# Kernel optimization log

Measured on AMD Instinct MI355X. Metric: run time of the kernel, lower is better.

## Reference

```python
import jax, jax.numpy as jnp
import numpy as np
import math

D = 128
LAMBDA_INIT = 0.8 - 0.6 * math.exp(-0.3 * 1)  # depth=1


def _clin(xr, xi, wr, wi, br, bi):
    # complex linear: (xr + i xi) @ (wr + i wi)^T + (br + i bi)
    o_r = jnp.einsum('bhsd,od->bhso', xr, wr) - jnp.einsum('bhsd,od->bhso', xi, wi) + br
    o_i = jnp.einsum('bhsd,od->bhso', xr, wi) + jnp.einsum('bhsd,od->bhso', xi, wr) + bi
    return o_r, o_i


def setup_inputs() -> dict:
    key = jax.random.key(0)
    ks = jax.random.split(key, 32)
    B, H, S = 1, 12, 1024
    shp = (B, H, S, D)
    inp = {}
    names = ['q_r', 'q_i', 'k_r', 'k_i', 'v_r', 'v_i', 'pe_q_r', 'pe_q_i', 'pe_k_r', 'pe_k_i']
    for i, n in enumerate(names):
        inp[n] = jax.random.normal(ks[i], shp, dtype=jnp.float32)
    std = 1.0 / math.sqrt(D)
    inp['qw_r'] = jax.random.normal(ks[10], (2 * D, D), jnp.float32) * std
    inp['qw_i'] = jax.random.normal(ks[11], (2 * D, D), jnp.float32) * std
    inp['qb_r'] = jnp.zeros((2 * D,), jnp.float32)
    inp['qb_i'] = jnp.zeros((2 * D,), jnp.float32)
    for j, p in enumerate(['k', 'v', 'g', 'o']):
        inp[p + 'w_r'] = jax.random.normal(ks[12 + 2 * j], (D, D), jnp.float32) * std
        inp[p + 'w_i'] = jax.random.normal(ks[13 + 2 * j], (D, D), jnp.float32) * std
        inp[p + 'b_r'] = jnp.zeros((D,), jnp.float32)
        inp[p + 'b_i'] = jnp.zeros((D,), jnp.float32)
    inp['lq1'] = jax.random.normal(ks[20], (D,), jnp.float32) * 0.1
    inp['lk1'] = jax.random.normal(ks[21], (D,), jnp.float32) * 0.1
    inp['lq2'] = jax.random.normal(ks[22], (D,), jnp.float32) * 0.1
    inp['lk2'] = jax.random.normal(ks[23], (D,), jnp.float32) * 0.1
    inp['sub_w'] = jnp.ones((2 * D,), jnp.float32)
    return inp


def _forward(q_r, q_i, k_r, k_i, v_r, v_i, pe_q_r, pe_q_i, pe_k_r, pe_k_i,
             qw_r, qw_i, qb_r, qb_i, kw_r, kw_i, kb_r, kb_i,
             vw_r, vw_i, vb_r, vb_i, gw_r, gw_i, gb_r, gb_i,
             ow_r, ow_i, ob_r, ob_i, lq1, lk1, lq2, lk2, sub_w):
    scale = D ** (-0.5)
    qp_r, qp_i = _clin(q_r, q_i, qw_r, qw_i, qb_r, qb_i)   # [B,H,S,2D]
    kp_r, kp_i = _clin(k_r, k_i, kw_r, kw_i, kb_r, kb_i)   # [B,H,S,D]
    vp_r, vp_i = _clin(v_r, v_i, vw_r, vw_i, vb_r, vb_i)
    qp_r = qp_r + jnp.concatenate([pe_q_r, pe_q_r], axis=-1)
    qp_i = qp_i + jnp.concatenate([pe_q_i, pe_q_i], axis=-1)
    kp_r = kp_r + pe_k_r
    kp_i = kp_i + pe_k_i
    q1_r, q2_r = jnp.split(qp_r, 2, axis=-1)
    q1_i, q2_i = jnp.split(qp_i, 2, axis=-1)

    def attn_w(qr, qi):
        s_r = jnp.einsum('bhqd,bhkd->bhqk', qr, kp_r) + jnp.einsum('bhqd,bhkd->bhqk', qi, kp_i)
        s_i = jnp.einsum('bhqd,bhkd->bhqk', qi, kp_r) - jnp.einsum('bhqd,bhkd->bhqk', qr, kp_i)
        mag = jnp.sqrt(s_r ** 2 + s_i ** 2 + 1e-8) * scale
        return jax.nn.softmax(mag.astype(jnp.float32), axis=-1).astype(s_r.dtype)

    w1 = attn_w(q1_r, q1_i)
    w2 = attn_w(q2_r, q2_i)
    a1_r = jnp.einsum('bhqk,bhkd->bhqd', w1, vp_r)
    a1_i = jnp.einsum('bhqk,bhkd->bhqd', w1, vp_i)
    a2_r = jnp.einsum('bhqk,bhkd->bhqd', w2, vp_r)
    a2_i = jnp.einsum('bhqk,bhkd->bhqd', w2, vp_i)
    cat_r = jnp.concatenate([a1_r, a2_r], axis=-1)
    cat_i = jnp.concatenate([a1_i, a2_i], axis=-1)
    rms = jnp.sqrt(jnp.mean(cat_r ** 2 + cat_i ** 2, axis=-1, keepdims=True) + 1e-5)
    cat_r = cat_r / rms * sub_w
    cat_i = cat_i / rms * sub_w
    a1_r, a2_r = jnp.split(cat_r, 2, axis=-1)
    a1_i, a2_i = jnp.split(cat_i, 2, axis=-1)
    lam1 = jnp.exp(jnp.sum(lq1 * lk1))
    lam2 = jnp.exp(jnp.sum(lq2 * lk2))
    lam = jax.nn.sigmoid(lam1 - lam2 + LAMBDA_INIT)
    out_r = a1_r - lam * a2_r
    out_i = a1_i - lam * a2_i
    g_r, g_i = _clin(q_r, q_i, gw_r, gw_i, gb_r, gb_i)
    out_r, out_i = g_r * out_r - g_i * out_i, g_r * out_i + g_i * out_r
    out_r, out_i = _clin(out_r, out_i, ow_r, ow_i, ob_r, ob_i)
    return out_r, out_i


def reference(q_r, q_i, k_r, k_i, v_r, v_i, pe_q_r, pe_q_i, pe_k_r, pe_k_i,
              qw_r, qw_i, qb_r, qb_i, kw_r, kw_i, kb_r, kb_i,
              vw_r, vw_i, vb_r, vb_i, gw_r, gw_i, gb_r, gb_i,
              ow_r, ow_i, ob_r, ob_i, lq1, lk1, lq2, lk2, sub_w):
    return _forward(q_r, q_i, k_r, k_i, v_r, v_i, pe_q_r, pe_q_i, pe_k_r, pe_k_i,
                    qw_r, qw_i, qb_r, qb_i, kw_r, kw_i, kb_r, kb_i,
                    vw_r, vw_i, vb_r, vb_i, gw_r, gw_i, gb_r, gb_i,
                    ow_r, ow_i, ob_r, ob_i, lq1, lk1, lq2, lk2, sub_w)
```

## Files before the change

kernel.cpp:

```cpp
#include <hip/hip_runtime.h>
#include <math.h>

#define H 12
#define S 1024
#define D 128
#define NROWS (H * S)

typedef __attribute__((ext_vector_type(8))) _Float16 f16x8;
typedef __attribute__((ext_vector_type(4))) float f32x4;
typedef __attribute__((ext_vector_type(4))) int i32x4;

__device__ __forceinline__ short f2h(float f) {
    _Float16 h = (_Float16)f;
    return __builtin_bit_cast(short, h);
}
__device__ __forceinline__ f16x8 fneg8(f16x8 v) {
    i32x4 u = __builtin_bit_cast(i32x4, v);
    u ^= (int)0x80008000;
    return __builtin_bit_cast(f16x8, u);
}

#define WS_QP_R   0ULL
#define WS_QP_I   6291456ULL
#define WS_KP_R   12582912ULL
#define WS_KP_I   15728640ULL
#define WS_VPT_R  18874368ULL
#define WS_VPT_I  22020096ULL
#define WS_G_R    25165824ULL
#define WS_G_I    31457280ULL
#define WS_ACAT_R 37748736ULL
#define WS_ACAT_I 50331648ULL
#define WS_LAM    62914560ULL
#define WS_SC     62914816ULL
#define W16_PER_HEAD  4194304ULL

__global__ void lam_kernel(const float* __restrict__ lq1, const float* __restrict__ lk1,
                           const float* __restrict__ lq2, const float* __restrict__ lk2,
                           float* __restrict__ lam_out)
{
    int t = threadIdx.x;
    float p1 = lq1[t] * lk1[t];
    float p2 = lq2[t] * lk2[t];
    #pragma unroll
    for (int off = 32; off; off >>= 1) {
        p1 += __shfl_xor(p1, off);
        p2 += __shfl_xor(p2, off);
    }
    __shared__ float s1[2], s2[2];
    if ((t & 63) == 0) { s1[t >> 6] = p1; s2[t >> 6] = p2; }
    __syncthreads();
    if (t == 0) {
        float l1 = expf(s1[0] + s1[1]);
        float l2 = expf(s2[0] + s2[1]);
        float x = l1 - l2 + 0.3555090675909693f;
        lam_out[0] = 1.0f / (1.0f + expf(-x));
    }
}

template <int OMODE>
__global__ __launch_bounds__(256) void clin_mfma(
    const float* __restrict__ xr, const float* __restrict__ xi,
    const float* __restrict__ wr, const float* __restrict__ wi,
    const float* __restrict__ br, const float* __restrict__ bi,
    const float* __restrict__ per, const float* __restrict__ pei,
    void* __restrict__ outr_, void* __restrict__ outi_, int M)
{
    __shared__ short As[128 * 72], Brs[64 * 72], Bis[64 * 72];
    const int t = threadIdx.x;
    const int row0 = blockIdx.x * 128, col0 = blockIdx.y * 64;
    const int lane = t & 63, wid = t >> 6;
    const int wm = (wid >> 1) * 64, wn = (wid & 1) * 32;
    const int fm = lane & 15, fq = lane >> 4;
    f32x4 zero4 = {0.f, 0.f, 0.f, 0.f};
    f32x4 accr[4][2], acci[4][2];
    #pragma unroll
    for (int i = 0; i < 4; ++i)
        #pragma unroll
        for (int j = 0; j < 2; ++j) { accr[i][j] = zero4; acci[i][j] = zero4; }

    for (int c = 0; c < 4; ++c) {
        const bool hi = (c >= 2);
        const int kb = (c & 1) * 64;
        const float* Asrc = hi ? xi : xr;
        const float* Brsrc = hi ? wi : wr;
        const float* Bisrc = hi ? wr : wi;
        const float bsign = hi ? -1.0f : 1.0f;
        __syncthreads();
        #pragma unroll
        for (int it = 0; it < 8; ++it) {
            int lin = it * 256 + t;
            int r = lin >> 4, k4 = (lin & 15) * 4;
            float4 va = *(const float4*)&Asrc[(size_t)(row0 + r) * 128 + kb + k4];
            *(short4*)&As[r * 72 + k4] = make_short4(f2h(va.x), f2h(va.y), f2h(va.z), f2h(va.w));
        }
        #pragma unroll
        for (int it = 0; it < 4; ++it) {
            int lin = it * 256 + t;
            int r = lin >> 4, k4 = (lin & 15) * 4;
            float4 vr = *(const float4*)&Brsrc[(size_t)(col0 + r) * 128 + kb + k4];
            *(short4*)&Brs[r * 72 + k4] = make_short4(f2h(bsign * vr.x), f2h(bsign * vr.y),
                                                      f2h(bsign * vr.z), f2h(bsign * vr.w));
            float4 vi = *(const float4*)&Bisrc[(size_t)(col0 + r) * 128 + kb + k4];
            *(short4*)&Bis[r * 72 + k4] = make_short4(f2h(vi.x), f2h(vi.y), f2h(vi.z), f2h(vi.w));
        }
        __syncthreads();
        #pragma unroll
        for (int ks = 0; ks < 64; ks += 32) {
            f16x8 bfr[2], bfi[2];
            #pragma unroll
            for (int j = 0; j < 2; ++j) {
                bfr[j] = *(const f16x8*)&Brs[(wn + j * 16 + fm) * 72 + ks + fq * 8];
                bfi[j] = *(const f16x8*)&Bis[(wn + j * 16 + fm) * 72 + ks + fq * 8];
            }
            #pragma unroll
            for (int i = 0; i < 4; ++i) {
                f16x8 a = *(const f16x8*)&As[(wm + i * 16 + fm) * 72 + ks + fq * 8];
                #pragma unroll
                for (int j = 0; j < 2; ++j) {
                    accr[i][j] = __builtin_amdgcn_mfma_f32_16x16x32_f16(a, bfr[j], accr[i][j], 0, 0, 0);
                    acci[i][j] = __builtin_amdgcn_mfma_f32_16x16x32_f16(a, bfi[j], acci[i][j], 0, 0, 0);
                }
            }
        }
    }
    #pragma unroll
    for (int i = 0; i < 4; ++i)
        #pragma unroll
        for (int j = 0; j < 2; ++j) {
            int colc = col0 + wn + j * 16 + fm;
            float bbr = br[colc], bbi = bi[colc];
            if (OMODE == 2) {
                int rb = row0 + wm + i * 16 + fq * 4;
                int hq = rb >> 10, sq = rb & 1023;
                short4 o_r4 = make_short4(f2h(accr[i][j][0] + bbr), f2h(accr[i][j][1] + bbr),
                                          f2h(accr[i][j][2] + bbr), f2h(accr[i][j][3] + bbr));
                short4 o_i4 = make_short4(f2h(acci[i][j][0] + bbi), f2h(acci[i][j][1] + bbi),
                                          f2h(acci[i][j][2] + bbi), f2h(acci[i][j][3] + bbi));
                size_t ob = ((size_t)(hq * 128 + colc)) * 1024 + sq;
                *(short4*)&((short*)outr_)[ob] = o_r4;
                *(short4*)&((short*)outi_)[ob] = o_i4;
            } else {
                #pragma unroll
                for (int reg = 0; reg < 4; ++reg) {
                    int rr = row0 + wm + i * 16 + fq * 4 + reg;
                    float o_r = accr[i][j][reg] + bbr;
                    float o_i = acci[i][j][reg] + bbi;
                    if (per) {
                        o_r += per[(size_t)rr * 128 + (colc & 127)];
                        o_i += pei[(size_t)rr * 128 + (colc & 127)];
                    }
                    if (OMODE == 1) {
                        ((short*)outr_)[(size_t)rr * M + colc] = f2h(o_r);
                        ((short*)outi_)[(size_t)rr * M + colc] = f2h(o_i);
                    } else {
                        ((float*)outr_)[(size_t)rr * M + colc] = o_r;
                        ((float*)outi_)[(size_t)rr * M + colc] = o_i;
                    }
                }
            }
        }
}

__global__ __launch_bounds__(256) void score_mfma(
    const short* __restrict__ qp_r, const short* __restrict__ qp_i,
    const short* __restrict__ kp_r, const short* __restrict__ kp_i,
    short* __restrict__ w16, int h0)
{
    __shared__ short Qr[128 * 72], Qi[128 * 72], Kt[128 * 72];
    const int t = threadIdx.x;
    const int hh = blockIdx.z >> 1, map = blockIdx.z & 1;
    const int h = h0 + hh;
    const int q0 = blockIdx.x * 128, c0 = blockIdx.y * 128;
    const int lane = t & 63, wid = t >> 6;
    const int wm = (wid >> 1) * 64, wn = (wid & 1) * 64;
    const int fm = lane & 15, fq = lane >> 4;
    f32x4 zero4 = {0.f, 0.f, 0.f, 0.f};
    f32x4 sr[4][4], si[4][4];
    #pragma unroll
    for (int i = 0; i < 4; ++i)
        #pragma unroll
        for (int j = 0; j < 4; ++j) { sr[i][j] = zero4; si[i][j] = zero4; }

    for (int kb = 0; kb < 2; ++kb) {
        const int kbase = map * 128 + kb * 64;
        __syncthreads();
        #pragma unroll
        for (int it = 0; it < 8; ++it) {
            int lin = it * 256 + t;
            int r = lin >> 4, k4 = (lin & 15) * 4;
            size_t qb = (size_t)(h * S + q0 + r) * 256 + kbase + k4;
            *(short4*)&Qr[r * 72 + k4] = *(const short4*)&qp_r[qb];
            *(short4*)&Qi[r * 72 + k4] = *(const short4*)&qp_i[qb];
            *(short4*)&Kt[r * 72 + k4] =
                *(const short4*)&kp_r[(size_t)(h * S + c0 + r) * 128 + kb * 64 + k4];
        }
        __syncthreads();
        #pragma unroll
        for (int ks = 0; ks < 64; ks += 32) {
            f16x8 b[4];
            #pragma unroll
            for (int j = 0; j < 4; ++j)
                b[j] = *(const f16x8*)&Kt[(wn + j * 16 + fm) * 72 + ks + fq * 8];
            #pragma unroll
            for (int i = 0; i < 4; ++i) {
                int ao = (wm + i * 16 + fm) * 72 + ks + fq * 8;
                f16x8 ar = *(const f16x8*)&Qr[ao];
                f16x8 ai = *(const f16x8*)&Qi[ao];
                #pragma unroll
                for (int j = 0; j < 4; ++j) {
                    sr[i][j] = __builtin_amdgcn_mfma_f32_16x16x32_f16(ar, b[j], sr[i][j], 0, 0, 0);
                    si[i][j] = __builtin_amdgcn_mfma_f32_16x16x32_f16(ai, b[j], si[i][j], 0, 0, 0);
                }
            }
        }
        __syncthreads();
        #pragma unroll
        for (int it = 0; it < 8; ++it) {
            int lin = it * 256 + t;
            int r = lin >> 4, k4 = (lin & 15) * 4;
            *(short4*)&Kt[r * 72 + k4] =
                *(const short4*)&kp_i[(size_t)(h * S + c0 + r) * 128 + kb * 64 + k4];
        }
        __syncthreads();
        #pragma unroll
        for (int ks = 0; ks < 64; ks += 32) {
            f16x8 b[4];
            #pragma unroll
            for (int j = 0; j < 4; ++j)
                b[j] = *(const f16x8*)&Kt[(wn + j * 16 + fm) * 72 + ks + fq * 8];
            #pragma unroll
            for (int i = 0; i < 4; ++i) {
                int ao = (wm + i * 16 + fm) * 72 + ks + fq * 8;
                f16x8 ar = *(const f16x8*)&Qr[ao];
                f16x8 ai = *(const f16x8*)&Qi[ao];
                f16x8 nr = fneg8(ar);
                #pragma unroll
                for (int j = 0; j < 4; ++j) {
                    sr[i][j] = __builtin_amdgcn_mfma_f32_16x16x32_f16(ai, b[j], sr[i][j], 0, 0, 0);
                    si[i][j] = __builtin_amdgcn_mfma_f32_16x16x32_f16(nr, b[j], si[i][j], 0, 0, 0);
                }
            }
        }
    }
    const float scale = 0.08838834764831845f;
    #pragma unroll
    for (int i = 0; i < 4; ++i)
        #pragma unroll
        for (int j = 0; j < 4; ++j) {
            int kcol = c0 + wn + j * 16 + fm;
            #pragma unroll
            for (int reg = 0; reg < 4; ++reg) {
                int q = q0 + wm + i * 16 + fq * 4 + reg;
                float r1 = sr[i][j][reg], I1 = si[i][j][reg];
                float m1 = sqrtf(fmaf(r1, r1, fmaf(I1, I1, 1e-8f))) * scale;
                w16[(((size_t)hh * 2 + map) * S + q) * S + kcol] = f2h(m1);
            }
        }
}

__global__ __launch_bounds__(256) void softmax_f16(short* __restrict__ w16)
{
    short* row = w16 + (size_t)blockIdx.x * S;
    int t = threadIdx.x;
    short4 s = ((short4*)row)[t];
    float f0 = (float)__builtin_bit_cast(_Float16, s.x);
    float f1 = (float)__builtin_bit_cast(_Float16, s.y);
    float f2v = (float)__builtin_bit_cast(_Float16, s.z);
    float f3 = (float)__builtin_bit_cast(_Float16, s.w);
    float m = fmaxf(fmaxf(f0, f1), fmaxf(f2v, f3));
    #pragma unroll
    for (int off = 32; off; off >>= 1) m = fmaxf(m, __shfl_xor(m, off));
    __shared__ float redm[4], reds[4];
    int w = t >> 6;
    if ((t & 63) == 0) redm[w] = m;
    __syncthreads();
    m = fmaxf(fmaxf(redm[0], redm[1]), fmaxf(redm[2], redm[3]));
    float e0 = __expf(f0 - m), e1 = __expf(f1 - m), e2 = __expf(f2v - m), e3 = __expf(f3 - m);
    float ssum = e0 + e1 + e2 + e3;
    #pragma unroll
    for (int off = 32; off; off >>= 1) ssum += __shfl_xor(ssum, off);
    if ((t & 63) == 0) reds[w] = ssum;
    __syncthreads();
    ssum = reds[0] + reds[1] + reds[2] + reds[3];
    float inv = 1.0f / ssum;
    s.x = f2h(e0 * inv); s.y = f2h(e1 * inv); s.z = f2h(e2 * inv); s.w = f2h(e3 * inv);
    ((short4*)row)[t] = s;
}

__global__ __launch_bounds__(256) void av_mfma(
    const short* __restrict__ w16, const short* __restrict__ vpT_r, const short* __restrict__ vpT_i,
    float* __restrict__ acat_r, float* __restrict__ acat_i, int h0)
{
    __shared__ short W1[64 * 72], W2[64 * 72], Vc[128 * 72];
    const int t = threadIdx.x;
    const int hh = blockIdx.z, h = h0 + hh;
    const int comp = blockIdx.y;
    const int q0 = blockIdx.x * 64;
    const short* vpT = comp ? vpT_i : vpT_r;
    float* acat = comp ? acat_i : acat_r;
    const int lane = t & 63, wid = t >> 6;
    const int wm = (wid >> 1) * 32, wn = (wid & 1) * 64;
    const int fm = lane & 15, fq = lane >> 4;
    f32x4 zero4 = {0.f, 0.f, 0.f, 0.f};
    f32x4 a1[2][4], a2[2][4];
    #pragma unroll
    for (int i = 0; i < 2; ++i)
        #pragma unroll
        for (int j = 0; j < 4; ++j) { a1[i][j] = zero4; a2[i][j] = zero4; }

    for (int k0 = 0; k0 < S; k0 += 64) {
        __syncthreads();
        #pragma unroll
        for (int it = 0; it < 4; ++it) {
            int lin = it * 256 + t;
            int r = lin >> 4, k4 = (lin & 15) * 4;
            *(short4*)&W1[r * 72 + k4] = *(const short4*)&w16[(((size_t)hh * 2 + 0) * S + q0 + r) * S + k0 + k4];
            *(short4*)&W2[r * 72 + k4] = *(const short4*)&w16[(((size_t)hh * 2 + 1) * S + q0 + r) * S + k0 + k4];
        }
        #pragma unroll
        for (int it = 0; it < 8; ++it) {
            int lin = it * 256 + t;
            int dd = lin >> 4, k4 = (lin & 15) * 4;
            *(short4*)&Vc[dd * 72 + k4] = *(const short4*)&vpT[(size_t)(h * 128 + dd) * 1024 + k0 + k4];
        }
        __syncthreads();
        #pragma unroll
        for (int ks = 0; ks < 64; ks += 32) {
            f16x8 b[4];
            #pragma unroll
            for (int j = 0; j < 4; ++j)
                b[j] = *(const f16x8*)&Vc[(wn + j * 16 + fm) * 72 + ks + fq * 8];
            #pragma unroll
            for (int i = 0; i < 2; ++i) {
                int wo = (wm + i * 16 + fm) * 72 + ks + fq * 8;
                f16x8 w1f = *(const f16x8*)&W1[wo];
                f16x8 w2f = *(const f16x8*)&W2[wo];
                #pragma unroll
                for (int j = 0; j < 4; ++j) {
                    a1[i][j] = __builtin_amdgcn_mfma_f32_16x16x32_f16(w1f, b[j], a1[i][j], 0, 0, 0);
                    a2[i][j] = __builtin_amdgcn_mfma_f32_16x16x32_f16(w2f, b[j], a2[i][j], 0, 0, 0);
                }
            }
        }
    }
    #pragma unroll
    for (int i = 0; i < 2; ++i)
        #pragma unroll
        for (int j = 0; j < 4; ++j) {
            int d = wn + j * 16 + fm;
            #pragma unroll
            for (int reg = 0; reg < 4; ++reg) {
                int q = q0 + wm + i * 16 + fq * 4 + reg;
                size_t rowb = (size_t)(h * S + q) * 256;
                acat[rowb + d]       = a1[i][j][reg];
                acat[rowb + 128 + d] = a2[i][j][reg];
            }
        }
}

__global__ __launch_bounds__(256) void rmsgate_kernel(
    const float* __restrict__ acat_r, const float* __restrict__ acat_i,
    const float* __restrict__ sub_w, const float* __restrict__ lam_ptr,
    float* __restrict__ g_r, float* __restrict__ g_i)
{
    int row = blockIdx.x;
    int t = threadIdx.x;
    float ar = acat_r[(size_t)row * 256 + t];
    float ai = acat_i[(size_t)row * 256 + t];
    float ss = fmaf(ar, ar, ai * ai);
    #pragma unroll
    for (int off = 32; off; off >>= 1) ss += __shfl_xor(ss, off);
    __shared__ float red[4];
    if ((t & 63) == 0) red[t >> 6] = ss;
    __syncthreads();
    float total = red[0] + red[1] + red[2] + red[3];
    float inv_rms = 1.0f / sqrtf(total * (1.0f / 256.0f) + 1e-5f);
    float sw = sub_w[t];
    __shared__ float Cr[256], Ci[256];
    Cr[t] = ar * inv_rms * sw;
    Ci[t] = ai * inv_rms * sw;
    __syncthreads();
    if (t < 128) {
        float lam = lam_ptr[0];
        float o_r = Cr[t] - lam * Cr[t + 128];
        float o_i = Ci[t] - lam * Ci[t + 128];
        float gr = g_r[(size_t)row * 128 + t];
        float gi = g_i[(size_t)row * 128 + t];
        g_r[(size_t)row * 128 + t] = gr * o_r - gi * o_i;
        g_i[(size_t)row * 128 + t] = gr * o_i + gi * o_r;
    }
}

extern "C" void kernel_launch(void* const* d_in, const int* in_sizes, int n_in,
                              void* d_out, int out_size, void* d_ws, size_t ws_size,
                              hipStream_t stream)
{
    (void)in_sizes; (void)n_in; (void)out_size;
    const float* q_r    = (const float*)d_in[0];
    const float* q_i    = (const float*)d_in[1];
    const float* k_r    = (const float*)d_in[2];
    const float* k_i    = (const float*)d_in[3];
    const float* v_r    = (const float*)d_in[4];
    const float* v_i    = (const float*)d_in[5];
    const float* pe_q_r = (const float*)d_in[6];
    const float* pe_q_i = (const float*)d_in[7];
    const float* pe_k_r = (const float*)d_in[8];
    const float* pe_k_i = (const float*)d_in[9];
    const float* qw_r   = (const float*)d_in[10];
    const float* qw_i   = (const float*)d_in[11];
    const float* qb_r   = (const float*)d_in[12];
    const float* qb_i   = (const float*)d_in[13];
    const float* kw_r   = (const float*)d_in[14];
    const float* kw_i   = (const float*)d_in[15];
    const float* kb_r   = (const float*)d_in[16];
    const float* kb_i   = (const float*)d_in[17];
    const float* vw_r   = (const float*)d_in[18];
    const float* vw_i   = (const float*)d_in[19];
    const float* vb_r   = (const float*)d_in[20];
    const float* vb_i   = (const float*)d_in[21];
    const float* gw_r   = (const float*)d_in[22];
    const float* gw_i   = (const float*)d_in[23];
    const float* gb_r   = (const float*)d_in[24];
    const float* gb_i   = (const float*)d_in[25];
    const float* ow_r   = (const float*)d_in[26];
    const float* ow_i   = (const float*)d_in[27];
    const float* ob_r   = (const float*)d_in[28];
    const float* ob_i   = (const float*)d_in[29];
    const float* lq1    = (const float*)d_in[30];
    const float* lk1    = (const float*)d_in[31];
    const float* lq2    = (const float*)d_in[32];
    const float* lk2    = (const float*)d_in[33];
    const float* sub_w  = (const float*)d_in[34];

    char* ws = (char*)d_ws;
    short* qp_r   = (short*)(ws + WS_QP_R);
    short* qp_i   = (short*)(ws + WS_QP_I);
    short* kp_r   = (short*)(ws + WS_KP_R);
    short* kp_i   = (short*)(ws + WS_KP_I);
    short* vpT_r  = (short*)(ws + WS_VPT_R);
    short* vpT_i  = (short*)(ws + WS_VPT_I);
    float* g_r    = (float*)(ws + WS_G_R);
    float* g_i    = (float*)(ws + WS_G_I);
    float* acat_r = (float*)(ws + WS_ACAT_R);
    float* acat_i = (float*)(ws + WS_ACAT_I);
    float* lam    = (float*)(ws + WS_LAM);
    short* w16    = (short*)(ws + WS_SC);

    float* out_r = (float*)d_out;
    float* out_i = out_r + (size_t)NROWS * D;

    size_t avail = ws_size > WS_SC ? ws_size - WS_SC : 0;
    int nh_chunk = (int)(avail / W16_PER_HEAD);
    if (nh_chunk < 1) nh_chunk = 1;
    if (nh_chunk > H) nh_chunk = H;

    lam_kernel<<<1, 128, 0, stream>>>(lq1, lk1, lq2, lk2, lam);

    clin_mfma<1><<<dim3(96, 4), 256, 0, stream>>>(q_r, q_i, qw_r, qw_i, qb_r, qb_i,
                                                  pe_q_r, pe_q_i, qp_r, qp_i, 256);
    clin_mfma<1><<<dim3(96, 2), 256, 0, stream>>>(k_r, k_i, kw_r, kw_i, kb_r, kb_i,
                                                  pe_k_r, pe_k_i, kp_r, kp_i, 128);
    clin_mfma<2><<<dim3(96, 2), 256, 0, stream>>>(v_r, v_i, vw_r, vw_i, vb_r, vb_i,
                                                  nullptr, nullptr, vpT_r, vpT_i, 128);
    clin_mfma<0><<<dim3(96, 2), 256, 0, stream>>>(q_r, q_i, gw_r, gw_i, gb_r, gb_i,
                                                  nullptr, nullptr, g_r, g_i, 128);

    for (int h0 = 0; h0 < H; h0 += nh_chunk) {
        int nhh = (H - h0 < nh_chunk) ? (H - h0) : nh_chunk;
        score_mfma<<<dim3(8, 8, nhh * 2), 256, 0, stream>>>(qp_r, qp_i, kp_r, kp_i, w16, h0);
        softmax_f16<<<nhh * 2 * S, 256, 0, stream>>>(w16);
        av_mfma<<<dim3(16, 2, nhh), 256, 0, stream>>>(w16, vpT_r, vpT_i, acat_r, acat_i, h0);
    }

    rmsgate_kernel<<<NROWS, 256, 0, stream>>>(acat_r, acat_i, sub_w, lam, g_r, g_i);

    clin_mfma<0><<<dim3(96, 2), 256, 0, stream>>>(g_r, g_i, ow_r, ow_i, ob_r, ob_i,
                                                  nullptr, nullptr, out_r, out_i, 128);
}
```

Before: 349.0 us.

## Merge input projections into one launch and halve score tile rows

Fuses the four complex input projections (q, k, v, gate) into one kernel whose grid y-index selects the operand set, so 960 blocks run in one launch instead of four smaller ones. The score kernel's query tile shrinks from 128 to 64 rows, doubling the block count and cutting accumulator registers, and Q fragments are now loaded into registers once per k-chunk and reused for both the real and imaginary K passes. The cost is runtime branching on the output mode inside the projection kernel and more K-tile reloads across score blocks.

```diff
diff --git a/kernel.cpp b/kernel.cpp
--- a/kernel.cpp
+++ b/kernel.cpp
@@ -57,17 +57,45 @@
     }
 }
 
-template <int OMODE>
-__global__ __launch_bounds__(256) void clin_mfma(
-    const float* __restrict__ xr, const float* __restrict__ xi,
-    const float* __restrict__ wr, const float* __restrict__ wi,
-    const float* __restrict__ br, const float* __restrict__ bi,
-    const float* __restrict__ per, const float* __restrict__ pei,
-    void* __restrict__ outr_, void* __restrict__ outi_, int M)
-{
+__global__ __launch_bounds__(256) void proj_all(
+    const float* __restrict__ q_r, const float* __restrict__ q_i,
+    const float* __restrict__ k_r, const float* __restrict__ k_i,
+    const float* __restrict__ v_r, const float* __restrict__ v_i,
+    const float* __restrict__ pe_q_r, const float* __restrict__ pe_q_i,
+    const float* __restrict__ pe_k_r, const float* __restrict__ pe_k_i,
+    const float* __restrict__ qw_r, const float* __restrict__ qw_i,
+    const float* __restrict__ qb_r, const float* __restrict__ qb_i,
+    const float* __restrict__ kw_r, const float* __restrict__ kw_i,
+    const float* __restrict__ kb_r, const float* __restrict__ kb_i,
+    const float* __restrict__ vw_r, const float* __restrict__ vw_i,
+    const float* __restrict__ vb_r, const float* __restrict__ vb_i,
+    const float* __restrict__ gw_r, const float* __restrict__ gw_i,
+    const float* __restrict__ gb_r, const float* __restrict__ gb_i,
+    short* __restrict__ qp_r, short* __restrict__ qp_i,
+    short* __restrict__ kp_r, short* __restrict__ kp_i,
+    short* __restrict__ vpT_r, short* __restrict__ vpT_i,
+    float* __restrict__ g_r, float* __restrict__ g_i)
+{
+    const int y = blockIdx.y;
+    const float *xr, *xi, *wr, *wi, *br, *bi, *per = nullptr, *pei = nullptr;
+    void *outr_, *outi_;
+    int M, omode, col0;
+    if (y < 4)      { xr = q_r; xi = q_i; wr = qw_r; wi = qw_i; br = qb_r; bi = qb_i;
+                      per = pe_q_r; pei = pe_q_i; outr_ = qp_r; outi_ = qp_i;
+                      M = 256; omode = 1; col0 = y * 64; }
+    else if (y < 6) { xr = k_r; xi = k_i; wr = kw_r; wi = kw_i; br = kb_r; bi = kb_i;
+                      per = pe_k_r; pei = pe_k_i; outr_ = kp_r; outi_ = kp_i;
+                      M = 128; omode = 1; col0 = (y - 4) * 64; }
+    else if (y < 8) { xr = v_r; xi = v_i; wr = vw_r; wi = vw_i; br = vb_r; bi = vb_i;
+                      outr_ = vpT_r; outi_ = vpT_i;
+                      M = 128; omode = 2; col0 = (y - 6) * 64; }
+    else            { xr = q_r; xi = q_i; wr = gw_r; wi = gw_i; br = gb_r; bi = gb_i;
+                      outr_ = g_r; outi_ = g_i;
+                      M = 128; omode = 0; col0 = (y - 8) * 64; }
+
     __shared__ short As[128 * 72], Brs[64 * 72], Bis[64 * 72];
     const int t = threadIdx.x;
-    const int row0 = blockIdx.x * 128, col0 = blockIdx.y * 64;
+    const int row0 = blockIdx.x * 128;
     const int lane = t & 63, wid = t >> 6;
     const int wm = (wid >> 1) * 64, wn = (wid & 1) * 32;
     const int fm = lane & 15, fq = lane >> 4;
@@ -129,7 +157,7 @@
         for (int j = 0; j < 2; ++j) {
             int colc = col0 + wn + j * 16 + fm;
             float bbr = br[colc], bbi = bi[colc];
-            if (OMODE == 2) {
+            if (omode == 2) {
                 int rb = row0 + wm + i * 16 + fq * 4;
                 int hq = rb >> 10, sq = rb & 1023;
                 short4 o_r4 = make_short4(f2h(accr[i][j][0] + bbr), f2h(accr[i][j][1] + bbr),
@@ -149,7 +177,7 @@
                         o_r += per[(size_t)rr * 128 + (colc & 127)];
                         o_i += pei[(size_t)rr * 128 + (colc & 127)];
                     }
-                    if (OMODE == 1) {
+                    if (omode == 1) {
                         ((short*)outr_)[(size_t)rr * M + colc] = f2h(o_r);
                         ((short*)outi_)[(size_t)rr * M + colc] = f2h(o_i);
                     } else {
@@ -161,23 +189,102 @@
         }
 }
 
+__global__ __launch_bounds__(256) void oproj_mfma(
+    const float* __restrict__ xr, const float* __restrict__ xi,
+    const float* __restrict__ wr, const float* __restrict__ wi,
+    const float* __restrict__ br, const float* __restrict__ bi,
+    float* __restrict__ outr, float* __restrict__ outi)
+{
+    __shared__ short As[128 * 72], Brs[64 * 72], Bis[64 * 72];
+    const int t = threadIdx.x;
+    const int row0 = blockIdx.x * 128, col0 = blockIdx.y * 64;
+    const int lane = t & 63, wid = t >> 6;
+    const int wm = (wid >> 1) * 64, wn = (wid & 1) * 32;
+    const int fm = lane & 15, fq = lane >> 4;
+    f32x4 zero4 = {0.f, 0.f, 0.f, 0.f};
+    f32x4 accr[4][2], acci[4][2];
+    #pragma unroll
+    for (int i = 0; i < 4; ++i)
+        #pragma unroll
+        for (int j = 0; j < 2; ++j) { accr[i][j] = zero4; acci[i][j] = zero4; }
+
+    for (int c = 0; c < 4; ++c) {
+        const bool hi = (c >= 2);
+        const int kb = (c & 1) * 64;
+        const float* Asrc = hi ? xi : xr;
+        const float* Brsrc = hi ? wi : wr;
+        const float* Bisrc = hi ? wr : wi;
+        const float bsign = hi ? -1.0f : 1.0f;
+        __syncthreads();
+        #pragma unroll
+        for (int it = 0; it < 8; ++it) {
+            int lin = it * 256 + t;
+            int r = lin >> 4, k4 = (lin & 15) * 4;
+            float4 va = *(const float4*)&Asrc[(size_t)(row0 + r) * 128 + kb + k4];
+            *(short4*)&As[r * 72 + k4] = make_short4(f2h(va.x), f2h(va.y), f2h(va.z), f2h(va.w));
+        }
+        #pragma unroll
+        for (int it = 0; it < 4; ++it) {
+            int lin = it * 256 + t;
+            int r = lin >> 4, k4 = (lin & 15) * 4;
+            float4 vr = *(const float4*)&Brsrc[(size_t)(col0 + r) * 128 + kb + k4];
+            *(short4*)&Brs[r * 72 + k4] = make_short4(f2h(bsign * vr.x), f2h(bsign * vr.y),
+                                                      f2h(bsign * vr.z), f2h(bsign * vr.w));
+            float4 vi = *(const float4*)&Bisrc[(size_t)(col0 + r) * 128 + kb + k4];
+            *(short4*)&Bis[r * 72 + k4] = make_short4(f2h(vi.x), f2h(vi.y), f2h(vi.z), f2h(vi.w));
+        }
+        __syncthreads();
+        #pragma unroll
+        for (int ks = 0; ks < 64; ks += 32) {
+            f16x8 bfr[2], bfi[2];
+            #pragma unroll
+            for (int j = 0; j < 2; ++j) {
+                bfr[j] = *(const f16x8*)&Brs[(wn + j * 16 + fm) * 72 + ks + fq * 8];
+                bfi[j] = *(const f16x8*)&Bis[(wn + j * 16 + fm) * 72 + ks + fq * 8];
+            }
+            #pragma unroll
+            for (int i = 0; i < 4; ++i) {
+                f16x8 a = *(const f16x8*)&As[(wm + i * 16 + fm) * 72 + ks + fq * 8];
+                #pragma unroll
+                for (int j = 0; j < 2; ++j) {
+                    accr[i][j] = __builtin_amdgcn_mfma_f32_16x16x32_f16(a, bfr[j], accr[i][j], 0, 0, 0);
+                    acci[i][j] = __builtin_amdgcn_mfma_f32_16x16x32_f16(a, bfi[j], acci[i][j], 0, 0, 0);
+                }
+            }
+        }
+    }
+    #pragma unroll
+    for (int i = 0; i < 4; ++i)
+        #pragma unroll
+        for (int j = 0; j < 2; ++j) {
+            int colc = col0 + wn + j * 16 + fm;
+            float bbr = br[colc], bbi = bi[colc];
+            #pragma unroll
+            for (int reg = 0; reg < 4; ++reg) {
+                int rr = row0 + wm + i * 16 + fq * 4 + reg;
+                outr[(size_t)rr * 128 + colc] = accr[i][j][reg] + bbr;
+                outi[(size_t)rr * 128 + colc] = acci[i][j][reg] + bbi;
+            }
+        }
+}
+
 __global__ __launch_bounds__(256) void score_mfma(
     const short* __restrict__ qp_r, const short* __restrict__ qp_i,
     const short* __restrict__ kp_r, const short* __restrict__ kp_i,
     short* __restrict__ w16, int h0)
 {
-    __shared__ short Qr[128 * 72], Qi[128 * 72], Kt[128 * 72];
+    __shared__ short Qr[64 * 72], Qi[64 * 72], Kt[128 * 72];
     const int t = threadIdx.x;
     const int hh = blockIdx.z >> 1, map = blockIdx.z & 1;
     const int h = h0 + hh;
-    const int q0 = blockIdx.x * 128, c0 = blockIdx.y * 128;
+    const int q0 = blockIdx.x * 64, c0 = blockIdx.y * 128;
     const int lane = t & 63, wid = t >> 6;
-    const int wm = (wid >> 1) * 64, wn = (wid & 1) * 64;
+    const int wm = (wid >> 1) * 32, wn = (wid & 1) * 64;
     const int fm = lane & 15, fq = lane >> 4;
     f32x4 zero4 = {0.f, 0.f, 0.f, 0.f};
-    f32x4 sr[4][4], si[4][4];
-    #pragma unroll
-    for (int i = 0; i < 4; ++i)
+    f32x4 sr[2][4], si[2][4];
+    #pragma unroll
+    for (int i = 0; i < 2; ++i)
         #pragma unroll
         for (int j = 0; j < 4; ++j) { sr[i][j] = zero4; si[i][j] = zero4; }
 
@@ -185,66 +292,72 @@
         const int kbase = map * 128 + kb * 64;
         __syncthreads();
         #pragma unroll
-        for (int it = 0; it < 8; ++it) {
-            int lin = it * 256 + t;
+        for (int i = 0; i < 4; ++i) {
+            int lin = i * 256 + t;
             int r = lin >> 4, k4 = (lin & 15) * 4;
             size_t qb = (size_t)(h * S + q0 + r) * 256 + kbase + k4;
             *(short4*)&Qr[r * 72 + k4] = *(const short4*)&qp_r[qb];
             *(short4*)&Qi[r * 72 + k4] = *(const short4*)&qp_i[qb];
+        }
+        #pragma unroll
+        for (int i = 0; i < 8; ++i) {
+            int lin = i * 256 + t;
+            int r = lin >> 4, k4 = (lin & 15) * 4;
             *(short4*)&Kt[r * 72 + k4] =
                 *(const short4*)&kp_r[(size_t)(h * S + c0 + r) * 128 + kb * 64 + k4];
         }
         __syncthreads();
-        #pragma unroll
-        for (int ks = 0; ks < 64; ks += 32) {
+        f16x8 aR[2][2], aI[2][2];
+        #pragma unroll
+        for (int ks = 0; ks < 2; ++ks)
+            #pragma unroll
+            for (int i = 0; i < 2; ++i) {
+                int ao = (wm + i * 16 + fm) * 72 + ks * 32 + fq * 8;
+                aR[ks][i] = *(const f16x8*)&Qr[ao];
+                aI[ks][i] = *(const f16x8*)&Qi[ao];
+            }
+        #pragma unroll
+        for (int ks = 0; ks < 2; ++ks) {
             f16x8 b[4];
             #pragma unroll
             for (int j = 0; j < 4; ++j)
-                b[j] = *(const f16x8*)&Kt[(wn + j * 16 + fm) * 72 + ks + fq * 8];
-            #pragma unroll
-            for (int i = 0; i < 4; ++i) {
-                int ao = (wm + i * 16 + fm) * 72 + ks + fq * 8;
-                f16x8 ar = *(const f16x8*)&Qr[ao];
-                f16x8 ai = *(const f16x8*)&Qi[ao];
+                b[j] = *(const f16x8*)&Kt[(wn + j * 16 + fm) * 72 + ks * 32 + fq * 8];
+            #pragma unroll
+            for (int i = 0; i < 2; ++i)
                 #pragma unroll
                 for (int j = 0; j < 4; ++j) {
-                    sr[i][j] = __builtin_amdgcn_mfma_f32_16x16x32_f16(ar, b[j], sr[i][j], 0, 0, 0);
-                    si[i][j] = __builtin_amdgcn_mfma_f32_16x16x32_f16(ai, b[j], si[i][j], 0, 0, 0);
+                    sr[i][j] = __builtin_amdgcn_mfma_f32_16x16x32_f16(aR[ks][i], b[j], sr[i][j], 0, 0, 0);
+                    si[i][j] = __builtin_amdgcn_mfma_f32_16x16x32_f16(aI[ks][i], b[j], si[i][j], 0, 0, 0);
                 }
-            }
-        }
-        __syncthreads();
-        #pragma unroll
-        for (int it = 0; it < 8; ++it) {
-            int lin = it * 256 + t;
+        }
+        __syncthreads();
+        #pragma unroll
+        for (int i = 0; i < 8; ++i) {
+            int lin = i * 256 + t;
             int r = lin >> 4, k4 = (lin & 15) * 4;
             *(short4*)&Kt[r * 72 + k4] =
                 *(const short4*)&kp_i[(size_t)(h * S + c0 + r) * 128 + kb * 64 + k4];
         }
         __syncthreads();
         #pragma unroll
-        for (int ks = 0; ks < 64; ks += 32) {
+        for (int ks = 0; ks < 2; ++ks) {
             f16x8 b[4];
             #pragma unroll
             for (int j = 0; j < 4; ++j)
-                b[j] = *(const f16x8*)&Kt[(wn + j * 16 + fm) * 72 + ks + fq * 8];
-            #pragma unroll
-            for (int i = 0; i < 4; ++i) {
-                int ao = (wm + i * 16 + fm) * 72 + ks + fq * 8;
-                f16x8 ar = *(const f16x8*)&Qr[ao];
-                f16x8 ai = *(const f16x8*)&Qi[ao];
-                f16x8 nr = fneg8(ar);
-                #pragma unroll
-                for (int j = 0; j < 4; ++j) {
-                    sr[i][j] = __builtin_amdgcn_mfma_f32_16x16x32_f16(ai, b[j], sr[i][j], 0, 0, 0);
-                    si[i][j] = __builtin_amdgcn_mfma_f32_16x16x32_f16(nr, b[j], si[i][j], 0, 0, 0);
-                }
+                b[j] = *(const f16x8*)&Kt[(wn + j * 16 + fm) * 72 + ks * 32 + fq * 8];
+            f16x8 nR0 = fneg8(aR[ks][0]), nR1 = fneg8(aR[ks][1]);
+            #pragma unroll
+            for (int j = 0; j < 4; ++j) {
+                sr[0][j] = __builtin_amdgcn_mfma_f32_16x16x32_f16(aI[ks][0], b[j], sr[0][j], 0, 0, 0);
+                si[0][j] = __builtin_amdgcn_mfma_f32_16x16x32_f16(nR0, b[j], si[0][j], 0, 0, 0);
+                sr[1][j] = __builtin_amdgcn_mfma_f32_16x16x32_f16(aI[ks][1], b[j], sr[1][j], 0, 0, 0);
+                si[1][j] = __builtin_amdgcn_mfma_f32_16x16x32_f16(nR1, b[j], si[1][j], 0, 0, 0);
             }
         }
     }
     const float scale = 0.08838834764831845f;
     #pragma unroll
-    for (int i = 0; i < 4; ++i)
+    for (int i = 0; i < 2; ++i)
         #pragma unroll
         for (int j = 0; j < 4; ++j) {
             int kcol = c0 + wn + j * 16 + fm;
@@ -456,24 +569,20 @@
 
     lam_kernel<<<1, 128, 0, stream>>>(lq1, lk1, lq2, lk2, lam);
 
-    clin_mfma<1><<<dim3(96, 4), 256, 0, stream>>>(q_r, q_i, qw_r, qw_i, qb_r, qb_i,
-                                                  pe_q_r, pe_q_i, qp_r, qp_i, 256);
-    clin_mfma<1><<<dim3(96, 2), 256, 0, stream>>>(k_r, k_i, kw_r, kw_i, kb_r, kb_i,
-                                                  pe_k_r, pe_k_i, kp_r, kp_i, 128);
-    clin_mfma<2><<<dim3(96, 2), 256, 0, stream>>>(v_r, v_i, vw_r, vw_i, vb_r, vb_i,
-                                                  nullptr, nullptr, vpT_r, vpT_i, 128);
-    clin_mfma<0><<<dim3(96, 2), 256, 0, stream>>>(q_r, q_i, gw_r, gw_i, gb_r, gb_i,
-                                                  nullptr, nullptr, g_r, g_i, 128);
+    proj_all<<<dim3(96, 10), 256, 0, stream>>>(
+        q_r, q_i, k_r, k_i, v_r, v_i, pe_q_r, pe_q_i, pe_k_r, pe_k_i,
+        qw_r, qw_i, qb_r, qb_i, kw_r, kw_i, kb_r, kb_i,
+        vw_r, vw_i, vb_r, vb_i, gw_r, gw_i, gb_r, gb_i,
+        qp_r, qp_i, kp_r, kp_i, vpT_r, vpT_i, g_r, g_i);
 
     for (int h0 = 0; h0 < H; h0 += nh_chunk) {
         int nhh = (H - h0 < nh_chunk) ? (H - h0) : nh_chunk;
-        score_mfma<<<dim3(8, 8, nhh * 2), 256, 0, stream>>>(qp_r, qp_i, kp_r, kp_i, w16, h0);
+        score_mfma<<<dim3(16, 8, nhh * 2), 256, 0, stream>>>(qp_r, qp_i, kp_r, kp_i, w16, h0);
         softmax_f16<<<nhh * 2 * S, 256, 0, stream>>>(w16);
         av_mfma<<<dim3(16, 2, nhh), 256, 0, stream>>>(w16, vpT_r, vpT_i, acat_r, acat_i, h0);
     }
 
     rmsgate_kernel<<<NROWS, 256, 0, stream>>>(acat_r, acat_i, sub_w, lam, g_r, g_i);
 
-    clin_mfma<0><<<dim3(96, 2), 256, 0, stream>>>(g_r, g_i, ow_r, ow_i, ob_r, ob_i,
-                                                  nullptr, nullptr, out_r, out_i, 128);
-}
+    oproj_mfma<<<dim3(96, 2), 256, 0, stream>>>(g_r, g_i, ow_r, ow_i, ob_r, ob_i, out_r, out_i);
+}
```

New measurement: 318.3 us. -8.8%, faster.
